# Performance work log

Measured on AMD Instinct MI355X. Metric: run time of the kernel, lower is better.

Reference implementation:

```python
import jax, jax.numpy as jnp
import numpy as np

B, D, H = 8, 512, 8
HD = D // H            # 64 head dim
NS, NT = 8192, 4096    # search / template points
ATTN_EPS = 1e-6
LN_EPS = 1e-5


def layer_norm(x, g, b):
    m = jnp.mean(x, axis=-1, keepdims=True)
    v = jnp.mean((x - m) ** 2, axis=-1, keepdims=True)
    return (x - m) * jax.lax.rsqrt(v + LN_EPS) * g + b


def setup_inputs() -> dict:
    key = jax.random.key(0)
    ks = jax.random.split(key, 20)
    s = 0.02
    return {
        "search_feat": jax.random.normal(ks[0], (B, D, NS), jnp.float32),
        "search_xyz": jax.random.uniform(ks[1], (B, NS, 3), jnp.float32),
        "template_feat": jax.random.normal(ks[2], (B, D, NT), jnp.float32),
        "template_xyz": jax.random.uniform(ks[3], (B, NT, 3), jnp.float32),
        "pos_w1": jax.random.normal(ks[4], (3, D), jnp.float32) * s,
        "pos_b1": jnp.zeros((D,), jnp.float32),
        "pos_w2": jax.random.normal(ks[5], (D, D), jnp.float32) * s,
        "pos_b2": jnp.zeros((D,), jnp.float32),
        "wq": jax.random.normal(ks[6], (D, D), jnp.float32) * s,
        "wk": jax.random.normal(ks[7], (D, D), jnp.float32) * s,
        "wv": jax.random.normal(ks[8], (D, D), jnp.float32) * s,
        "w_merge": jax.random.normal(ks[9], (D, D), jnp.float32) * s,
        "mlp_w1": jax.random.normal(ks[10], (2 * D, 2 * D), jnp.float32) * s,
        "mlp_w2": jax.random.normal(ks[11], (2 * D, D), jnp.float32) * s,
        "ln1_g": jnp.ones((D,), jnp.float32),
        "ln1_b": jnp.zeros((D,), jnp.float32),
        "ln2_g": jnp.ones((D,), jnp.float32),
        "ln2_b": jnp.zeros((D,), jnp.float32),
    }


def reference(search_feat, search_xyz, template_feat, template_xyz,
              pos_w1, pos_b1, pos_w2, pos_b2, wq, wk, wv, w_merge,
              mlp_w1, mlp_w2, ln1_g, ln1_b, ln2_g, ln2_b):
    bs = search_feat.shape[0]
    sf = jnp.transpose(search_feat, (0, 2, 1))    # [B, Ns, D]
    tf = jnp.transpose(template_feat, (0, 2, 1))  # [B, Nt, D]

    # positional MLP on template coordinates
    pos = jax.nn.relu(template_xyz @ pos_w1 + pos_b1) @ pos_w2 + pos_b2
    tf_pos = tf + pos

    q = (sf @ wq).reshape(bs, NS, H, HD)
    k = (tf @ wk).reshape(bs, NT, H, HD)
    v = (tf_pos @ wv).reshape(bs, NT, H, HD)

    # LoFTR-style linear attention: phi(x) = elu(x) + 1
    Q = jax.nn.elu(q) + 1.0
    K = jax.nn.elu(k) + 1.0
    v_len = v.shape[1]
    v_n = v / v_len
    KV = jnp.einsum("bshd,bshv->bhdv", K, v_n)                 # [B,H,d,d]
    Z = 1.0 / (jnp.einsum("blhd,bhd->blh", Q, K.sum(axis=1)) + ATTN_EPS)
    msg = jnp.einsum("blhd,bhdv->blhv", Q, KV) * Z[..., None] * v_len

    msg = msg.reshape(bs, NS, H * HD) @ w_merge
    msg = layer_norm(msg, ln1_g, ln1_b)
    cat = jnp.concatenate([sf, msg], axis=2)                    # [B,Ns,2D]
    msg = jax.nn.relu(cat @ mlp_w1) @ mlp_w2
    msg = layer_norm(msg, ln2_g, ln2_b)
    return jnp.transpose(sf + msg, (0, 2, 1))                   # [B,D,Ns]
```

## Files before the change

kernel.cpp:

```cpp
#include <hip/hip_runtime.h>
#include <stdint.h>
#include <stddef.h>


using ushort_t = unsigned short;
using short8 = __attribute__((ext_vector_type(8))) short;
using f32x4  = __attribute__((ext_vector_type(4))) float;

#define DEVI __device__ __forceinline__

DEVI float b2f(unsigned short u) {
    unsigned v = ((unsigned)u) << 16;
    return __builtin_bit_cast(float, v);
}
DEVI unsigned short f2b(float x) {
    unsigned u = __builtin_bit_cast(unsigned, x);
    u += 0x7FFFu + ((u >> 16) & 1u);
    return (unsigned short)(u >> 16);
}
DEVI void gload16(const void* g, void* l) {
    __builtin_amdgcn_global_load_lds(
        (const __attribute__((address_space(1))) unsigned*)g,
        (__attribute__((address_space(3))) unsigned*)l, 16, 0, 0);
}

template <int EPI>
__global__ __launch_bounds__(512, 2)
void gemm_bf16(const ushort_t* __restrict__ A0, const ushort_t* __restrict__ A1,
               const ushort_t* __restrict__ Wt, ushort_t* __restrict__ C,
               const float* __restrict__ bias, const ushort_t* __restrict__ addm,
               int N, int K, int K0, int lda0, int lda1, int nn)
{
    __shared__ ushort_t As[2][256 * 64];
    __shared__ ushort_t Bs[2][256 * 64];
    const int tid = threadIdx.x;
    const int cpx = gridDim.x >> 3;
    const int lid = (blockIdx.x & 7) * cpx + (blockIdx.x >> 3);
    const int m0 = (lid / nn) * 256;
    const int n0 = (lid % nn) * 256;
    const int w = tid >> 6, l = tid & 63;
    const int wm = (w >> 2) * 128;
    const int wn = (w & 3) * 64;
    const int lr = l & 15, lg = l >> 4;
    const int srow = tid >> 3;
    const int sck  = (tid & 7) ^ (srow & 7);
    const int nk = K / 64;

    f32x4 accA[4][4] = {};
    f32x4 accB[4][4] = {};

    auto stageA = [&](int kt, int buf) {
        const int kb = kt * 64;
        const ushort_t* p; int ld;
        if (kb < K0) { p = A0 + (size_t)m0 * lda0 + kb; ld = lda0; }
        else         { p = A1 + (size_t)m0 * lda1 + (kb - K0); ld = lda1; }
        p += (size_t)srow * ld + sck * 8;
#pragma unroll
        for (int j = 0; j < 4; j++)
            gload16(p + (size_t)(j * 64) * ld,
                    (void*)(&As[buf][j * 4096] + tid * 8));
    };
    auto stageB = [&](int kt, int buf) {
        const ushort_t* p = Wt + (size_t)(n0 + srow) * K + kt * 64 + sck * 8;
#pragma unroll
        for (int j = 0; j < 4; j++)
            gload16(p + (size_t)(j * 64) * K,
                    (void*)(&Bs[buf][j * 4096] + tid * 8));
    };

    short8 aP[4], aQ[4], aR[4], b0[4], b1[4];

    auto ldA = [&](short8 (&dst)[4], int mh, int ks, int cb) {
#pragma unroll
        for (int mf = 0; mf < 4; mf++) {
            const int r = wm + mh * 64 + mf * 16 + lr;
            dst[mf] = *(const short8*)&As[cb][r * 64 + ((ks * 4 + lg) ^ (r & 7)) * 8];
        }
    };
    auto ldB = [&](short8 (&dst)[4], int ks, int cb) {
#pragma unroll
        for (int nf = 0; nf < 4; nf++) {
            const int r = wn + nf * 16 + lr;
            dst[nf] = *(const short8*)&Bs[cb][r * 64 + ((ks * 4 + lg) ^ (r & 7)) * 8];
        }
    };
    auto MM = [&](f32x4 (&ac)[4][4], short8 (&af)[4], short8 (&bf)[4]) {
        __builtin_amdgcn_s_setprio(1);
#pragma unroll
        for (int mf = 0; mf < 4; mf++)
#pragma unroll
            for (int nf = 0; nf < 4; nf++)
                ac[mf][nf] = __builtin_amdgcn_mfma_f32_16x16x32_bf16(
                    af[mf], bf[nf], ac[mf][nf], 0, 0, 0);
        __builtin_amdgcn_s_setprio(0);
    };

    stageA(0, 0); stageB(0, 0);
    asm volatile("s_waitcnt vmcnt(0)" ::: "memory");
    __builtin_amdgcn_s_barrier();
    ldA(aP, 0, 0, 0); ldB(b0, 0, 0);

    for (int t = 0; t < nk; ++t) {
        const int cur = t & 1;
        const bool pre = (t + 1) < nk;
        ldA(aQ, 1, 0, cur); ldB(b1, 1, cur);
        if (pre) stageA(t + 1, cur ^ 1);
        MM(accA, aP, b0);
        ldA(aR, 0, 1, cur);
        if (pre) stageB(t + 1, cur ^ 1);
        MM(accB, aQ, b0);
        ldA(aP, 1, 1, cur);
        MM(accA, aR, b1);
        MM(accB, aP, b1);
        if (pre) {
            asm volatile("s_waitcnt vmcnt(0)" ::: "memory");
            __builtin_amdgcn_s_barrier();
            ldA(aP, 0, 0, cur ^ 1); ldB(b0, 0, cur ^ 1);
        }
    }

#pragma unroll
    for (int mf = 0; mf < 4; mf++) {
#pragma unroll
        for (int i = 0; i < 4; i++) {
            const int mA = m0 + wm + mf * 16 + lg * 4 + i;
            const int mB = mA + 64;
#pragma unroll
            for (int nf = 0; nf < 4; nf++) {
                const int n = n0 + wn + nf * 16 + lr;
                float x = accA[mf][nf][i];
                float y = accB[mf][nf][i];
                if constexpr (EPI == 1) {
                    x = x > 0.f ? x + 1.f : __expf(x);
                    y = y > 0.f ? y + 1.f : __expf(y);
                }
                if constexpr (EPI == 2) {
                    x += bias[n] + b2f(addm[(size_t)mA * N + n]);
                    y += bias[n] + b2f(addm[(size_t)mB * N + n]);
                }
                if constexpr (EPI == 3) { x = fmaxf(x, 0.f); y = fmaxf(y, 0.f); }
                C[(size_t)mA * N + n] = f2b(x);
                C[(size_t)mB * N + n] = f2b(y);
            }
        }
    }
}

__global__ __launch_bounds__(512, 2)
void gemm_proj(const ushort_t* __restrict__ sfT, const ushort_t* __restrict__ tfT,
               const ushort_t* __restrict__ P1,
               const ushort_t* __restrict__ wqT, const ushort_t* __restrict__ wkT,
               const ushort_t* __restrict__ pw2T,
               ushort_t* __restrict__ Qp, ushort_t* __restrict__ Kp,
               ushort_t* __restrict__ tfpos, const float* __restrict__ pos_b2)
{
    __shared__ ushort_t As[2][256 * 64];
    __shared__ ushort_t Bs[2][256 * 64];
    const int tid = threadIdx.x;
    const int cpx = gridDim.x >> 3;
    const int lid = (blockIdx.x & 7) * cpx + (blockIdx.x >> 3);
    const ushort_t* A0; const ushort_t* Wt; ushort_t* C; int loc; bool doElu;
    if (lid < 512)      { loc = lid;       A0 = sfT; Wt = wqT;  C = Qp;    doElu = true; }
    else if (lid < 768) { loc = lid - 512; A0 = tfT; Wt = wkT;  C = Kp;    doElu = true; }
    else                { loc = lid - 768; A0 = P1;  Wt = pw2T; C = tfpos; doElu = false; }
    const int m0 = (loc >> 1) * 256;
    const int n0 = (loc & 1) * 256;
    const int w = tid >> 6, l = tid & 63;
    const int wm = (w >> 2) * 128;
    const int wn = (w & 3) * 64;
    const int lr = l & 15, lg = l >> 4;
    const int srow = tid >> 3;
    const int sck  = (tid & 7) ^ (srow & 7);
    const int nk = 8;

    f32x4 accA[4][4] = {};
    f32x4 accB[4][4] = {};

    auto stageA = [&](int kt, int buf) {
        const ushort_t* p = A0 + (size_t)(m0 + srow) * 512 + kt * 64 + sck * 8;
#pragma unroll
        for (int j = 0; j < 4; j++)
            gload16(p + (size_t)(j * 64) * 512,
                    (void*)(&As[buf][j * 4096] + tid * 8));
    };
    auto stageB = [&](int kt, int buf) {
        const ushort_t* p = Wt + (size_t)(n0 + srow) * 512 + kt * 64 + sck * 8;
#pragma unroll
        for (int j = 0; j < 4; j++)
            gload16(p + (size_t)(j * 64) * 512,
                    (void*)(&Bs[buf][j * 4096] + tid * 8));
    };

    short8 aP[4], aQ[4], aR[4], b0[4], b1[4];

    auto ldA = [&](short8 (&dst)[4], int mh, int ks, int cb) {
#pragma unroll
        for (int mf = 0; mf < 4; mf++) {
            const int r = wm + mh * 64 + mf * 16 + lr;
            dst[mf] = *(const short8*)&As[cb][r * 64 + ((ks * 4 + lg) ^ (r & 7)) * 8];
        }
    };
    auto ldB = [&](short8 (&dst)[4], int ks, int cb) {
#pragma unroll
        for (int nf = 0; nf < 4; nf++) {
            const int r = wn + nf * 16 + lr;
            dst[nf] = *(const short8*)&Bs[cb][r * 64 + ((ks * 4 + lg) ^ (r & 7)) * 8];
        }
    };
    auto MM = [&](f32x4 (&ac)[4][4], short8 (&af)[4], short8 (&bf)[4]) {
        __builtin_amdgcn_s_setprio(1);
#pragma unroll
        for (int mf = 0; mf < 4; mf++)
#pragma unroll
            for (int nf = 0; nf < 4; nf++)
                ac[mf][nf] = __builtin_amdgcn_mfma_f32_16x16x32_bf16(
                    af[mf], bf[nf], ac[mf][nf], 0, 0, 0);
        __builtin_amdgcn_s_setprio(0);
    };

    stageA(0, 0); stageB(0, 0);
    asm volatile("s_waitcnt vmcnt(0)" ::: "memory");
    __builtin_amdgcn_s_barrier();
    ldA(aP, 0, 0, 0); ldB(b0, 0, 0);

    for (int t = 0; t < nk; ++t) {
        const int cur = t & 1;
        const bool pre = (t + 1) < nk;
        ldA(aQ, 1, 0, cur); ldB(b1, 1, cur);
        if (pre) stageA(t + 1, cur ^ 1);
        MM(accA, aP, b0);
        ldA(aR, 0, 1, cur);
        if (pre) stageB(t + 1, cur ^ 1);
        MM(accB, aQ, b0);
        ldA(aP, 1, 1, cur);
        MM(accA, aR, b1);
        MM(accB, aP, b1);
        if (pre) {
            asm volatile("s_waitcnt vmcnt(0)" ::: "memory");
            __builtin_amdgcn_s_barrier();
            ldA(aP, 0, 0, cur ^ 1); ldB(b0, 0, cur ^ 1);
        }
    }

#pragma unroll
    for (int mf = 0; mf < 4; mf++) {
#pragma unroll
        for (int i = 0; i < 4; i++) {
            const int mA = m0 + wm + mf * 16 + lg * 4 + i;
            const int mB = mA + 64;
#pragma unroll
            for (int nf = 0; nf < 4; nf++) {
                const int n = n0 + wn + nf * 16 + lr;
                float x = accA[mf][nf][i];
                float y = accB[mf][nf][i];
                if (doElu) {
                    x = x > 0.f ? x + 1.f : __expf(x);
                    y = y > 0.f ? y + 1.f : __expf(y);
                } else {
                    x += pos_b2[n] + b2f(tfT[(size_t)mA * 512 + n]);
                    y += pos_b2[n] + b2f(tfT[(size_t)mB * 512 + n]);
                }
                C[(size_t)mA * 512 + n] = f2b(x);
                C[(size_t)mB * 512 + n] = f2b(y);
            }
        }
    }
}

__global__ __launch_bounds__(256)
void prep(const float* __restrict__ sfeat, const float* __restrict__ tfeat,
          const float* __restrict__ xyz, const float* __restrict__ pw1,
          const float* __restrict__ pb1,
          const float* wq, const float* wk, const float* wv, const float* wm,
          const float* pw2, const float* w1, const float* w2,
          ushort_t* sfT, ushort_t* tfT, ushort_t* P1,
          ushort_t* wqT, ushort_t* wkT, ushort_t* wvT, ushort_t* wmT,
          ushort_t* pw2T, ushort_t* w1T, ushort_t* w2T)
{
    const int bid = blockIdx.x;
    const int t = threadIdx.x;
    if (bid >= 12992) {
        const int m = (bid - 12992) * 4 + (t >> 6);
        const int n0 = (t & 63) * 8;
        const float x = xyz[m * 3 + 0], y = xyz[m * 3 + 1], z = xyz[m * 3 + 2];
        short8 o;
#pragma unroll
        for (int j = 0; j < 8; j++) {
            const int n = n0 + j;
            float v = x * pw1[n] + y * pw1[512 + n] + z * pw1[1024 + n] + pb1[n];
            o[j] = (short)f2b(fmaxf(v, 0.f));
        }
        *(short8*)&P1[(size_t)m * 512 + n0] = o;
        return;
    }
    __shared__ float tile[64][65];
    const float* src; ushort_t* dst; int R, Cc, c0, r0;
    if (bid < 8192) {
        const int b = bid >> 10, rem = bid & 1023;
        src = sfeat + (size_t)b * 512 * 8192; dst = sfT + (size_t)b * 512 * 8192;
        R = 512; Cc = 8192; c0 = (rem & 127) * 64; r0 = (rem >> 7) * 64;
    } else if (bid < 12288) {
        const int lcl = bid - 8192; const int b = lcl >> 9, rem = lcl & 511;
        src = tfeat + (size_t)b * 512 * 4096; dst = tfT + (size_t)b * 512 * 4096;
        R = 512; Cc = 4096; c0 = (rem & 63) * 64; r0 = (rem >> 6) * 64;
    } else {
        const int lcl = bid - 12288;
        if (lcl < 320) {
            const int wsel = lcl >> 6, local = lcl & 63;
            const float* srcs[5] = {wq, wk, wv, wm, pw2};
            ushort_t* dsts[5] = {wqT, wkT, wvT, wmT, pw2T};
            src = srcs[wsel]; dst = dsts[wsel];
            R = 512; Cc = 512; c0 = (local & 7) * 64; r0 = (local >> 3) * 64;
        } else if (lcl < 576) {
            const int local = lcl - 320;
            src = w1; dst = w1T; R = 1024; Cc = 1024;
            c0 = (local & 15) * 64; r0 = (local >> 4) * 64;
        } else {
            const int local = lcl - 576;
            src = w2; dst = w2T; R = 1024; Cc = 512;
            c0 = (local & 7) * 64; r0 = (local >> 3) * 64;
        }
    }
#pragma unroll
    for (int i = 0; i < 4; i++) {
        const int r = (t >> 4) + i * 16;
        const int c = (t & 15) * 4;
        const float4 v = *(const float4*)&src[(size_t)(r0 + r) * Cc + c0 + c];
        tile[r][c + 0] = v.x; tile[r][c + 1] = v.y;
        tile[r][c + 2] = v.z; tile[r][c + 3] = v.w;
    }
    __syncthreads();
#pragma unroll
    for (int i = 0; i < 2; i++) {
        const int c = (t >> 3) + i * 32;
        const int rs = (t & 7) * 8;
        short8 o;
#pragma unroll
        for (int j = 0; j < 8; j++) o[j] = (short)f2b(tile[rs + j][c]);
        *(short8*)&dst[(size_t)(c0 + c) * R + r0 + rs] = o;
    }
}

__global__ __launch_bounds__(256)
void kv_partial(const ushort_t* __restrict__ Kp, const ushort_t* __restrict__ V,
                float* __restrict__ KVp, float* __restrict__ Ksp)
{
    __shared__ ushort_t Ks[256 * 64];
    __shared__ ushort_t Vs[256 * 64];
    const int t = threadIdx.x;
    const int sp = blockIdx.x, h = blockIdx.y, b = blockIdx.z;
    const int d0 = t >> 2, e0 = (t & 3) * 16;
    const int srow = t >> 3, scol = (t & 7) * 8;
    float acc[16] = {};
    float ksum = 0.f;
    for (int c = 0; c < 2; c++) {
        if (c) __syncthreads();
        const size_t sbase = (size_t)b * 4096 + sp * 512 + c * 256;
#pragma unroll
        for (int i = 0; i < 8; i++) {
            const size_t go = (sbase + i * 32 + srow) * 512 + h * 64 + scol;
            gload16(Kp + go, (void*)(&Ks[i * 2048] + t * 8));
            gload16(V + go, (void*)(&Vs[i * 2048] + t * 8));
        }
        __syncthreads();
        for (int s = 0; s < 256; s++) {
            const float k = b2f(Ks[s * 64 + d0]);
            if ((t & 3) == 0) ksum += k;
            const short8 v0 = *(const short8*)&Vs[s * 64 + e0];
            const short8 v1 = *(const short8*)&Vs[s * 64 + e0 + 8];
#pragma unroll
            for (int j = 0; j < 8; j++) {
                acc[j]     += k * b2f((unsigned short)v0[j]);
                acc[8 + j] += k * b2f((unsigned short)v1[j]);
            }
        }
    }
    const int bh = b * 8 + h;
    float* kvo = KVp + (((size_t)sp * 64 + bh) * 64 + d0) * 64 + e0;
#pragma unroll
    for (int j = 0; j < 16; j++) kvo[j] = acc[j];
    if ((t & 3) == 0) Ksp[((size_t)sp * 64 + bh) * 64 + d0] = ksum;
}

__global__ __launch_bounds__(256)
void kv_finalize(const float* __restrict__ KVp, const float* __restrict__ Ksp,
                 ushort_t* __restrict__ KVt)
{
    const int bh = blockIdx.x, t = threadIdx.x;
    ushort_t* o = KVt + (size_t)bh * 5120;
#pragma unroll
    for (int i = 0; i < 16; i++) {
        const int idx = i * 256 + t;
        const int e = idx >> 6, d = idx & 63;
        float s = 0.f;
#pragma unroll
        for (int sp = 0; sp < 8; sp++)
            s += KVp[(((size_t)sp * 64 + bh) * 64 + d) * 64 + e];
        o[idx] = f2b(s);
    }
    if (t < 64) {
        float s = 0.f;
#pragma unroll
        for (int sp = 0; sp < 8; sp++) s += Ksp[((size_t)sp * 64 + bh) * 64 + t];
        o[4096 + t] = f2b(s);
    }
    for (int idx = 4160 + t; idx < 5120; idx += 256) o[idx] = 0;
}

__global__ __launch_bounds__(256, 2)
void attn_apply(const ushort_t* __restrict__ Qp, const ushort_t* __restrict__ KVt,
                ushort_t* __restrict__ msg1)
{
    __shared__ ushort_t As[256 * 64];
    __shared__ ushort_t Bs[80 * 64];
    const int t = threadIdx.x;
    const int ch = blockIdx.x, h = blockIdx.y, b = blockIdx.z;
    const int w = t >> 6, l = t & 63;
    const int lr = l & 15, lg = l >> 4;
    const int row0 = ch * 256;
    const int srow = t >> 3;
    const int sc = ((t & 7) ^ (srow & 7)) * 8;
    const ushort_t* kv = KVt + (size_t)(b * 8 + h) * 5120;
#pragma unroll
    for (int i = 0; i < 2; i++)
        gload16(kv + (size_t)(i * 32 + srow) * 64 + sc,
                (void*)(&Bs[i * 2048] + t * 8));
    if (t < 128)
        gload16(kv + (size_t)(64 + srow) * 64 + sc,
                (void*)(&Bs[4096] + t * 8));
    const ushort_t* qb = Qp + ((size_t)b * 8192 + row0) * 512 + h * 64;
#pragma unroll
    for (int i = 0; i < 8; i++)
        gload16(qb + (size_t)(i * 32 + srow) * 512 + sc,
                (void*)(&As[i * 2048] + t * 8));
    __syncthreads();
    f32x4 acc[4][5] = {};
    const int wr = w * 64;
#pragma unroll
    for (int ks = 0; ks < 2; ks++) {
        const int kswz = ((ks * 4 + lg) ^ (lr & 7)) * 8;
        short8 a[4], bb[5];
#pragma unroll
        for (int mf = 0; mf < 4; mf++)
            a[mf] = *(const short8*)&As[(wr + mf * 16 + lr) * 64 + kswz];
#pragma unroll
        for (int nf = 0; nf < 5; nf++)
            bb[nf] = *(const short8*)&Bs[(nf * 16 + lr) * 64 + kswz];
#pragma unroll
        for (int mf = 0; mf < 4; mf++)
#pragma unroll
            for (int nf = 0; nf < 5; nf++)
                acc[mf][nf] = __builtin_amdgcn_mfma_f32_16x16x32_bf16(
                    a[mf], bb[nf], acc[mf][nf], 0, 0, 0);
    }
#pragma unroll
    for (int mf = 0; mf < 4; mf++) {
#pragma unroll
        for (int i = 0; i < 4; i++) {
            const int m = row0 + wr + mf * 16 + lg * 4 + i;
            const float zden = __shfl(acc[mf][4][i], (l & 48));
            const float z = 1.f / (zden + 1e-6f);
#pragma unroll
            for (int nf = 0; nf < 4; nf++) {
                const int e = nf * 16 + lr;
                msg1[((size_t)b * 8192 + m) * 512 + h * 64 + e] =
                    f2b(acc[mf][nf][i] * z);
            }
        }
    }
}

__global__ __launch_bounds__(256)
void layer_norm_k(ushort_t* __restrict__ X, const float* __restrict__ g,
                  const float* __restrict__ bta)
{
    const int t = threadIdx.x;
    const int row = blockIdx.x * 4 + (t >> 6);
    const int l = t & 63;
    ushort_t* x = X + (size_t)row * 512;
    const short8 v = *(const short8*)&x[l * 8];
    float f[8];
    float s = 0.f;
#pragma unroll
    for (int j = 0; j < 8; j++) { f[j] = b2f((unsigned short)v[j]); s += f[j]; }
#pragma unroll
    for (int o = 32; o > 0; o >>= 1) s += __shfl_xor(s, o);
    const float mean = s * (1.f / 512.f);
    float vs = 0.f;
#pragma unroll
    for (int j = 0; j < 8; j++) { const float d = f[j] - mean; vs += d * d; }
#pragma unroll
    for (int o = 32; o > 0; o >>= 1) vs += __shfl_xor(vs, o);
    const float rstd = rsqrtf(vs * (1.f / 512.f) + 1e-5f);
    short8 ov;
#pragma unroll
    for (int j = 0; j < 8; j++) {
        const int c = l * 8 + j;
        ov[j] = (short)f2b((f[j] - mean) * rstd * g[c] + bta[c]);
    }
    *(short8*)&x[l * 8] = ov;
}

__global__ __launch_bounds__(256)
void ln2_final(const ushort_t* __restrict__ outp, const ushort_t* __restrict__ sfT,
               const float* __restrict__ g, const float* __restrict__ bta,
               float* __restrict__ out)
{
    __shared__ ushort_t tile[64][514];
    const int t = threadIdx.x;
    const int ns0 = blockIdx.x * 64, b = blockIdx.y;
    const int w = t >> 6, l = t & 63;
#pragma unroll
    for (int rr = 0; rr < 16; rr++) {
        const int r = w * 16 + rr;
        const size_t grow = (size_t)b * 8192 + ns0 + r;
        const short8 v = *(const short8*)&outp[grow * 512 + l * 8];
        float f[8];
        float s = 0.f;
#pragma unroll
        for (int j = 0; j < 8; j++) { f[j] = b2f((unsigned short)v[j]); s += f[j]; }
#pragma unroll
        for (int o = 32; o > 0; o >>= 1) s += __shfl_xor(s, o);
        const float mean = s * (1.f / 512.f);
        float vs = 0.f;
#pragma unroll
        for (int j = 0; j < 8; j++) { const float d = f[j] - mean; vs += d * d; }
#pragma unroll
        for (int o = 32; o > 0; o >>= 1) vs += __shfl_xor(vs, o);
        const float rstd = rsqrtf(vs * (1.f / 512.f) + 1e-5f);
        const short8 sv = *(const short8*)&sfT[grow * 512 + l * 8];
        short8 ov;
#pragma unroll
        for (int j = 0; j < 8; j++) {
            const int c = l * 8 + j;
            ov[j] = (short)f2b(b2f((unsigned short)sv[j]) +
                               (f[j] - mean) * rstd * g[c] + bta[c]);
        }
        *(short8*)&tile[r][l * 8] = ov;
    }
    __syncthreads();
#pragma unroll
    for (int i = 0; i < 32; i++) {
        const int d = (t >> 4) + i * 16;
        const int nss = (t & 15) * 4;
        float4 o;
        o.x = b2f(tile[nss + 0][d]);
        o.y = b2f(tile[nss + 1][d]);
        o.z = b2f(tile[nss + 2][d]);
        o.w = b2f(tile[nss + 3][d]);
        *(float4*)&out[((size_t)b * 512 + d) * 8192 + ns0 + nss] = o;
    }
}

extern "C" void kernel_launch(void* const* d_in, const int* in_sizes, int n_in,
                              void* d_out, int out_size, void* d_ws, size_t ws_size,
                              hipStream_t stream)
{
    (void)in_sizes; (void)n_in; (void)out_size; (void)ws_size;
    const float* search_feat   = (const float*)d_in[0];
    const float* template_feat = (const float*)d_in[2];
    const float* template_xyz  = (const float*)d_in[3];
    const float* pos_w1  = (const float*)d_in[4];
    const float* pos_b1  = (const float*)d_in[5];
    const float* pos_w2  = (const float*)d_in[6];
    const float* pos_b2  = (const float*)d_in[7];
    const float* wq      = (const float*)d_in[8];
    const float* wk      = (const float*)d_in[9];
    const float* wv      = (const float*)d_in[10];
    const float* w_merge = (const float*)d_in[11];
    const float* mlp_w1  = (const float*)d_in[12];
    const float* mlp_w2  = (const float*)d_in[13];
    const float* ln1_g   = (const float*)d_in[14];
    const float* ln1_b   = (const float*)d_in[15];
    const float* ln2_g   = (const float*)d_in[16];
    const float* ln2_b   = (const float*)d_in[17];
    float* out = (float*)d_out;

    char* ws = (char*)d_ws;
    ushort_t* sfT    = (ushort_t*)(ws + 0);
    ushort_t* Qp     = (ushort_t*)(ws + 67108864);
    ushort_t* tfT    = (ushort_t*)(ws + 134217728);
    ushort_t* Kp     = (ushort_t*)(ws + 167772160);
    ushort_t* msg2   = (ushort_t*)(ws + 134217728);
    ushort_t* P1     = (ushort_t*)(ws + 201326592);
    ushort_t* Vv     = (ushort_t*)(ws + 201326592);
    ushort_t* tfpos  = (ushort_t*)(ws + 234881024);
    ushort_t* msg1   = (ushort_t*)(ws + 268435456);
    ushort_t* hidden = (ushort_t*)(ws + 201326592);
    ushort_t* outp   = Qp;
    ushort_t* wqT  = (ushort_t*)(ws + 335544320);
    ushort_t* wkT  = (ushort_t*)(ws + 336068608);
    ushort_t* wvT  = (ushort_t*)(ws + 336592896);
    ushort_t* wmT  = (ushort_t*)(ws + 337117184);
    ushort_t* pw2T = (ushort_t*)(ws + 337641472);
    ushort_t* w1T  = (ushort_t*)(ws + 338165760);
    ushort_t* w2T  = (ushort_t*)(ws + 340262912);
    float*    KVp  = (float*)(ws + 268435456);
    float*    Ksp  = (float*)(ws + 276824064);
    ushort_t* KVt  = (ushort_t*)(ws + 345571328);

    prep<<<dim3(21184), 256, 0, stream>>>(
        search_feat, template_feat, template_xyz, pos_w1, pos_b1,
        wq, wk, wv, w_merge, pos_w2, mlp_w1, mlp_w2,
        sfT, tfT, P1, wqT, wkT, wvT, wmT, pw2T, w1T, w2T);
    gemm_proj<<<dim3(1024), 512, 0, stream>>>(sfT, tfT, P1, wqT, wkT, pw2T,
                                              Qp, Kp, tfpos, pos_b2);
    gemm_bf16<0><<<dim3(256), 512, 0, stream>>>(tfpos, nullptr, wvT, Vv,
                                                nullptr, nullptr, 512, 512, 512, 512, 0, 2);
    kv_partial<<<dim3(8, 8, 8), 256, 0, stream>>>(Kp, Vv, KVp, Ksp);
    kv_finalize<<<dim3(64), 256, 0, stream>>>(KVp, Ksp, KVt);
    attn_apply<<<dim3(32, 8, 8), 256, 0, stream>>>(Qp, KVt, msg1);
    gemm_bf16<0><<<dim3(512), 512, 0, stream>>>(msg1, nullptr, wmT, msg2,
                                                nullptr, nullptr, 512, 512, 512, 512, 0, 2);
    layer_norm_k<<<dim3(16384), 256, 0, stream>>>(msg2, ln1_g, ln1_b);
    gemm_bf16<3><<<dim3(1024), 512, 0, stream>>>(sfT, msg2, w1T, hidden,
                                                 nullptr, nullptr, 1024, 1024, 512, 512, 512, 4);
    gemm_bf16<0><<<dim3(512), 512, 0, stream>>>(hidden, nullptr, w2T, outp,
                                                nullptr, nullptr, 512, 1024, 1024, 1024, 0, 2);
    ln2_final<<<dim3(128, 8), 256, 0, stream>>>(outp, sfT, ln2_g, ln2_b, out);
}
```

Before: 708.1 us.

## Replace 256x256 double-buffered GEMMs with single-buffered 128x128 tiles

Every GEMM kernel, the fused projection one included, moves from 256x256 tiles with 512 threads and double-buffered LDS prefetch to 128x128 tiles with 256 threads and a single LDS buffer. Grids grow four- to eightfold and launch bounds now allow four blocks per CU. The aim is more parallelism and better wave occupancy for these fairly small GEMMs. In exchange, each tile does less operand reuse and global loads no longer overlap with MFMA work inside a block, so the code relies on other resident blocks to hide that latency.

```diff
diff --git a/kernel.cpp b/kernel.cpp
--- a/kernel.cpp
+++ b/kernel.cpp
@@ -25,128 +25,89 @@
 }
 
 template <int EPI>
-__global__ __launch_bounds__(512, 2)
-void gemm_bf16(const ushort_t* __restrict__ A0, const ushort_t* __restrict__ A1,
-               const ushort_t* __restrict__ Wt, ushort_t* __restrict__ C,
-               const float* __restrict__ bias, const ushort_t* __restrict__ addm,
-               int N, int K, int K0, int lda0, int lda1, int nn)
-{
-    __shared__ ushort_t As[2][256 * 64];
-    __shared__ ushort_t Bs[2][256 * 64];
+__global__ __launch_bounds__(256, 4)
+void gemm128(const ushort_t* __restrict__ A0, const ushort_t* __restrict__ A1,
+             const ushort_t* __restrict__ Wt, ushort_t* __restrict__ C,
+             const float* __restrict__ bias, const ushort_t* __restrict__ addm,
+             int N, int K, int K0, int lda0, int lda1, int nn)
+{
+    __shared__ ushort_t As[128 * 64];
+    __shared__ ushort_t Bs[128 * 64];
     const int tid = threadIdx.x;
     const int cpx = gridDim.x >> 3;
     const int lid = (blockIdx.x & 7) * cpx + (blockIdx.x >> 3);
-    const int m0 = (lid / nn) * 256;
-    const int n0 = (lid % nn) * 256;
+    const int m0 = (lid / nn) * 128;
+    const int n0 = (lid % nn) * 128;
     const int w = tid >> 6, l = tid & 63;
-    const int wm = (w >> 2) * 128;
-    const int wn = (w & 3) * 64;
+    const int wm = (w >> 1) * 64, wn = (w & 1) * 64;
     const int lr = l & 15, lg = l >> 4;
     const int srow = tid >> 3;
     const int sck  = (tid & 7) ^ (srow & 7);
     const int nk = K / 64;
 
-    f32x4 accA[4][4] = {};
-    f32x4 accB[4][4] = {};
-
-    auto stageA = [&](int kt, int buf) {
-        const int kb = kt * 64;
-        const ushort_t* p; int ld;
-        if (kb < K0) { p = A0 + (size_t)m0 * lda0 + kb; ld = lda0; }
-        else         { p = A1 + (size_t)m0 * lda1 + (kb - K0); ld = lda1; }
-        p += (size_t)srow * ld + sck * 8;
-#pragma unroll
-        for (int j = 0; j < 4; j++)
-            gload16(p + (size_t)(j * 64) * ld,
-                    (void*)(&As[buf][j * 4096] + tid * 8));
-    };
-    auto stageB = [&](int kt, int buf) {
-        const ushort_t* p = Wt + (size_t)(n0 + srow) * K + kt * 64 + sck * 8;
-#pragma unroll
-        for (int j = 0; j < 4; j++)
-            gload16(p + (size_t)(j * 64) * K,
-                    (void*)(&Bs[buf][j * 4096] + tid * 8));
-    };
-
-    short8 aP[4], aQ[4], aR[4], b0[4], b1[4];
-
-    auto ldA = [&](short8 (&dst)[4], int mh, int ks, int cb) {
-#pragma unroll
-        for (int mf = 0; mf < 4; mf++) {
-            const int r = wm + mh * 64 + mf * 16 + lr;
-            dst[mf] = *(const short8*)&As[cb][r * 64 + ((ks * 4 + lg) ^ (r & 7)) * 8];
-        }
-    };
-    auto ldB = [&](short8 (&dst)[4], int ks, int cb) {
-#pragma unroll
-        for (int nf = 0; nf < 4; nf++) {
-            const int r = wn + nf * 16 + lr;
-            dst[nf] = *(const short8*)&Bs[cb][r * 64 + ((ks * 4 + lg) ^ (r & 7)) * 8];
-        }
-    };
-    auto MM = [&](f32x4 (&ac)[4][4], short8 (&af)[4], short8 (&bf)[4]) {
-        __builtin_amdgcn_s_setprio(1);
-#pragma unroll
-        for (int mf = 0; mf < 4; mf++)
-#pragma unroll
-            for (int nf = 0; nf < 4; nf++)
-                ac[mf][nf] = __builtin_amdgcn_mfma_f32_16x16x32_bf16(
-                    af[mf], bf[nf], ac[mf][nf], 0, 0, 0);
-        __builtin_amdgcn_s_setprio(0);
-    };
-
-    stageA(0, 0); stageB(0, 0);
-    asm volatile("s_waitcnt vmcnt(0)" ::: "memory");
-    __builtin_amdgcn_s_barrier();
-    ldA(aP, 0, 0, 0); ldB(b0, 0, 0);
+    f32x4 acc[4][4] = {};
 
     for (int t = 0; t < nk; ++t) {
-        const int cur = t & 1;
-        const bool pre = (t + 1) < nk;
-        ldA(aQ, 1, 0, cur); ldB(b1, 1, cur);
-        if (pre) stageA(t + 1, cur ^ 1);
-        MM(accA, aP, b0);
-        ldA(aR, 0, 1, cur);
-        if (pre) stageB(t + 1, cur ^ 1);
-        MM(accB, aQ, b0);
-        ldA(aP, 1, 1, cur);
-        MM(accA, aR, b1);
-        MM(accB, aP, b1);
-        if (pre) {
-            asm volatile("s_waitcnt vmcnt(0)" ::: "memory");
-            __builtin_amdgcn_s_barrier();
-            ldA(aP, 0, 0, cur ^ 1); ldB(b0, 0, cur ^ 1);
-        }
+        const int kb = t * 64;
+        {
+            const ushort_t* p; int ld;
+            if (kb < K0) { p = A0 + (size_t)m0 * lda0 + kb; ld = lda0; }
+            else         { p = A1 + (size_t)m0 * lda1 + (kb - K0); ld = lda1; }
+            p += (size_t)srow * ld + sck * 8;
+#pragma unroll
+            for (int j = 0; j < 4; j++)
+                gload16(p + (size_t)(j * 32) * ld, (void*)(&As[j * 2048] + tid * 8));
+            const ushort_t* q = Wt + (size_t)(n0 + srow) * K + kb + sck * 8;
+#pragma unroll
+            for (int j = 0; j < 4; j++)
+                gload16(q + (size_t)(j * 32) * K, (void*)(&Bs[j * 2048] + tid * 8));
+        }
+        asm volatile("s_waitcnt vmcnt(0)" ::: "memory");
+        __builtin_amdgcn_s_barrier();
+#pragma unroll
+        for (int ks = 0; ks < 2; ks++) {
+            short8 a[4], b[4];
+#pragma unroll
+            for (int mf = 0; mf < 4; mf++) {
+                const int r = wm + mf * 16 + lr;
+                a[mf] = *(const short8*)&As[r * 64 + ((ks * 4 + lg) ^ (r & 7)) * 8];
+            }
+#pragma unroll
+            for (int nf = 0; nf < 4; nf++) {
+                const int r = wn + nf * 16 + lr;
+                b[nf] = *(const short8*)&Bs[r * 64 + ((ks * 4 + lg) ^ (r & 7)) * 8];
+            }
+            __builtin_amdgcn_s_setprio(1);
+#pragma unroll
+            for (int mf = 0; mf < 4; mf++)
+#pragma unroll
+                for (int nf = 0; nf < 4; nf++)
+                    acc[mf][nf] = __builtin_amdgcn_mfma_f32_16x16x32_bf16(
+                        a[mf], b[nf], acc[mf][nf], 0, 0, 0);
+            __builtin_amdgcn_s_setprio(0);
+        }
+        __builtin_amdgcn_s_barrier();
     }
 
 #pragma unroll
     for (int mf = 0; mf < 4; mf++) {
 #pragma unroll
         for (int i = 0; i < 4; i++) {
-            const int mA = m0 + wm + mf * 16 + lg * 4 + i;
-            const int mB = mA + 64;
+            const int m = m0 + wm + mf * 16 + lg * 4 + i;
 #pragma unroll
             for (int nf = 0; nf < 4; nf++) {
                 const int n = n0 + wn + nf * 16 + lr;
-                float x = accA[mf][nf][i];
-                float y = accB[mf][nf][i];
-                if constexpr (EPI == 1) {
-                    x = x > 0.f ? x + 1.f : __expf(x);
-                    y = y > 0.f ? y + 1.f : __expf(y);
-                }
-                if constexpr (EPI == 2) {
-                    x += bias[n] + b2f(addm[(size_t)mA * N + n]);
-                    y += bias[n] + b2f(addm[(size_t)mB * N + n]);
-                }
-                if constexpr (EPI == 3) { x = fmaxf(x, 0.f); y = fmaxf(y, 0.f); }
-                C[(size_t)mA * N + n] = f2b(x);
-                C[(size_t)mB * N + n] = f2b(y);
-            }
-        }
-    }
-}
-
-__global__ __launch_bounds__(512, 2)
+                float x = acc[mf][nf][i];
+                if constexpr (EPI == 1) { x = x > 0.f ? x + 1.f : __expf(x); }
+                if constexpr (EPI == 2) { x += bias[n] + b2f(addm[(size_t)m * N + n]); }
+                if constexpr (EPI == 3) { x = fmaxf(x, 0.f); }
+                C[(size_t)m * N + n] = f2b(x);
+            }
+        }
+    }
+}
+
+__global__ __launch_bounds__(256, 4)
 void gemm_proj(const ushort_t* __restrict__ sfT, const ushort_t* __restrict__ tfT,
                const ushort_t* __restrict__ P1,
                const ushort_t* __restrict__ wqT, const ushort_t* __restrict__ wkT,
@@ -154,114 +115,79 @@
                ushort_t* __restrict__ Qp, ushort_t* __restrict__ Kp,
                ushort_t* __restrict__ tfpos, const float* __restrict__ pos_b2)
 {
-    __shared__ ushort_t As[2][256 * 64];
-    __shared__ ushort_t Bs[2][256 * 64];
+    __shared__ ushort_t As[128 * 64];
+    __shared__ ushort_t Bs[128 * 64];
     const int tid = threadIdx.x;
     const int cpx = gridDim.x >> 3;
     const int lid = (blockIdx.x & 7) * cpx + (blockIdx.x >> 3);
     const ushort_t* A0; const ushort_t* Wt; ushort_t* C; int loc; bool doElu;
-    if (lid < 512)      { loc = lid;       A0 = sfT; Wt = wqT;  C = Qp;    doElu = true; }
-    else if (lid < 768) { loc = lid - 512; A0 = tfT; Wt = wkT;  C = Kp;    doElu = true; }
-    else                { loc = lid - 768; A0 = P1;  Wt = pw2T; C = tfpos; doElu = false; }
-    const int m0 = (loc >> 1) * 256;
-    const int n0 = (loc & 1) * 256;
+    if (lid < 2048)      { loc = lid;        A0 = sfT; Wt = wqT;  C = Qp;    doElu = true; }
+    else if (lid < 3072) { loc = lid - 2048; A0 = tfT; Wt = wkT;  C = Kp;    doElu = true; }
+    else                 { loc = lid - 3072; A0 = P1;  Wt = pw2T; C = tfpos; doElu = false; }
+    const int m0 = (loc >> 2) * 128;
+    const int n0 = (loc & 3) * 128;
     const int w = tid >> 6, l = tid & 63;
-    const int wm = (w >> 2) * 128;
-    const int wn = (w & 3) * 64;
+    const int wm = (w >> 1) * 64, wn = (w & 1) * 64;
     const int lr = l & 15, lg = l >> 4;
     const int srow = tid >> 3;
     const int sck  = (tid & 7) ^ (srow & 7);
-    const int nk = 8;
-
-    f32x4 accA[4][4] = {};
-    f32x4 accB[4][4] = {};
-
-    auto stageA = [&](int kt, int buf) {
-        const ushort_t* p = A0 + (size_t)(m0 + srow) * 512 + kt * 64 + sck * 8;
-#pragma unroll
-        for (int j = 0; j < 4; j++)
-            gload16(p + (size_t)(j * 64) * 512,
-                    (void*)(&As[buf][j * 4096] + tid * 8));
-    };
-    auto stageB = [&](int kt, int buf) {
-        const ushort_t* p = Wt + (size_t)(n0 + srow) * 512 + kt * 64 + sck * 8;
-#pragma unroll
-        for (int j = 0; j < 4; j++)
-            gload16(p + (size_t)(j * 64) * 512,
-                    (void*)(&Bs[buf][j * 4096] + tid * 8));
-    };
-
-    short8 aP[4], aQ[4], aR[4], b0[4], b1[4];
-
-    auto ldA = [&](short8 (&dst)[4], int mh, int ks, int cb) {
-#pragma unroll
-        for (int mf = 0; mf < 4; mf++) {
-            const int r = wm + mh * 64 + mf * 16 + lr;
-            dst[mf] = *(const short8*)&As[cb][r * 64 + ((ks * 4 + lg) ^ (r & 7)) * 8];
-        }
-    };
-    auto ldB = [&](short8 (&dst)[4], int ks, int cb) {
-#pragma unroll
-        for (int nf = 0; nf < 4; nf++) {
-            const int r = wn + nf * 16 + lr;
-            dst[nf] = *(const short8*)&Bs[cb][r * 64 + ((ks * 4 + lg) ^ (r & 7)) * 8];
-        }
-    };
-    auto MM = [&](f32x4 (&ac)[4][4], short8 (&af)[4], short8 (&bf)[4]) {
-        __builtin_amdgcn_s_setprio(1);
-#pragma unroll
-        for (int mf = 0; mf < 4; mf++)
-#pragma unroll
-            for (int nf = 0; nf < 4; nf++)
-                ac[mf][nf] = __builtin_amdgcn_mfma_f32_16x16x32_bf16(
-                    af[mf], bf[nf], ac[mf][nf], 0, 0, 0);
-        __builtin_amdgcn_s_setprio(0);
-    };
-
-    stageA(0, 0); stageB(0, 0);
-    asm volatile("s_waitcnt vmcnt(0)" ::: "memory");
-    __builtin_amdgcn_s_barrier();
-    ldA(aP, 0, 0, 0); ldB(b0, 0, 0);
-
-    for (int t = 0; t < nk; ++t) {
-        const int cur = t & 1;
-        const bool pre = (t + 1) < nk;
-        ldA(aQ, 1, 0, cur); ldB(b1, 1, cur);
-        if (pre) stageA(t + 1, cur ^ 1);
-        MM(accA, aP, b0);
-        ldA(aR, 0, 1, cur);
-        if (pre) stageB(t + 1, cur ^ 1);
-        MM(accB, aQ, b0);
-        ldA(aP, 1, 1, cur);
-        MM(accA, aR, b1);
-        MM(accB, aP, b1);
-        if (pre) {
-            asm volatile("s_waitcnt vmcnt(0)" ::: "memory");
-            __builtin_amdgcn_s_barrier();
-            ldA(aP, 0, 0, cur ^ 1); ldB(b0, 0, cur ^ 1);
-        }
+
+    f32x4 acc[4][4] = {};
+
+    for (int t = 0; t < 8; ++t) {
+        const int kb = t * 64;
+        {
+            const ushort_t* p = A0 + (size_t)(m0 + srow) * 512 + kb + sck * 8;
+#pragma unroll
+            for (int j = 0; j < 4; j++)
+                gload16(p + (size_t)(j * 32) * 512, (void*)(&As[j * 2048] + tid * 8));
+            const ushort_t* q = Wt + (size_t)(n0 + srow) * 512 + kb + sck * 8;
+#pragma unroll
+            for (int j = 0; j < 4; j++)
+                gload16(q + (size_t)(j * 32) * 512, (void*)(&Bs[j * 2048] + tid * 8));
+        }
+        asm volatile("s_waitcnt vmcnt(0)" ::: "memory");
+        __builtin_amdgcn_s_barrier();
+#pragma unroll
+        for (int ks = 0; ks < 2; ks++) {
+            short8 a[4], b[4];
+#pragma unroll
+            for (int mf = 0; mf < 4; mf++) {
+                const int r = wm + mf * 16 + lr;
+                a[mf] = *(const short8*)&As[r * 64 + ((ks * 4 + lg) ^ (r & 7)) * 8];
+            }
+#pragma unroll
+            for (int nf = 0; nf < 4; nf++) {
+                const int r = wn + nf * 16 + lr;
+                b[nf] = *(const short8*)&Bs[r * 64 + ((ks * 4 + lg) ^ (r & 7)) * 8];
+            }
+            __builtin_amdgcn_s_setprio(1);
+#pragma unroll
+            for (int mf = 0; mf < 4; mf++)
+#pragma unroll
+                for (int nf = 0; nf < 4; nf++)
+                    acc[mf][nf] = __builtin_amdgcn_mfma_f32_16x16x32_bf16(
+                        a[mf], b[nf], acc[mf][nf], 0, 0, 0);
+            __builtin_amdgcn_s_setprio(0);
+        }
+        __builtin_amdgcn_s_barrier();
     }
 
 #pragma unroll
     for (int mf = 0; mf < 4; mf++) {
 #pragma unroll
         for (int i = 0; i < 4; i++) {
-            const int mA = m0 + wm + mf * 16 + lg * 4 + i;
-            const int mB = mA + 64;
+            const int m = m0 + wm + mf * 16 + lg * 4 + i;
 #pragma unroll
             for (int nf = 0; nf < 4; nf++) {
                 const int n = n0 + wn + nf * 16 + lr;
-                float x = accA[mf][nf][i];
-                float y = accB[mf][nf][i];
+                float x = acc[mf][nf][i];
                 if (doElu) {
                     x = x > 0.f ? x + 1.f : __expf(x);
-                    y = y > 0.f ? y + 1.f : __expf(y);
                 } else {
-                    x += pos_b2[n] + b2f(tfT[(size_t)mA * 512 + n]);
-                    y += pos_b2[n] + b2f(tfT[(size_t)mB * 512 + n]);
+                    x += pos_b2[n] + b2f(tfT[(size_t)m * 512 + n]);
                 }
-                C[(size_t)mA * 512 + n] = f2b(x);
-                C[(size_t)mB * 512 + n] = f2b(y);
+                C[(size_t)m * 512 + n] = f2b(x);
             }
         }
     }
@@ -603,19 +529,19 @@
         search_feat, template_feat, template_xyz, pos_w1, pos_b1,
         wq, wk, wv, w_merge, pos_w2, mlp_w1, mlp_w2,
         sfT, tfT, P1, wqT, wkT, wvT, wmT, pw2T, w1T, w2T);
-    gemm_proj<<<dim3(1024), 512, 0, stream>>>(sfT, tfT, P1, wqT, wkT, pw2T,
+    gemm_proj<<<dim3(4096), 256, 0, stream>>>(sfT, tfT, P1, wqT, wkT, pw2T,
                                               Qp, Kp, tfpos, pos_b2);
-    gemm_bf16<0><<<dim3(256), 512, 0, stream>>>(tfpos, nullptr, wvT, Vv,
-                                                nullptr, nullptr, 512, 512, 512, 512, 0, 2);
+    gemm128<0><<<dim3(1024), 256, 0, stream>>>(tfpos, nullptr, wvT, Vv,
+                                               nullptr, nullptr, 512, 512, 512, 512, 0, 4);
     kv_partial<<<dim3(8, 8, 8), 256, 0, stream>>>(Kp, Vv, KVp, Ksp);
     kv_finalize<<<dim3(64), 256, 0, stream>>>(KVp, Ksp, KVt);
     attn_apply<<<dim3(32, 8, 8), 256, 0, stream>>>(Qp, KVt, msg1);
-    gemm_bf16<0><<<dim3(512), 512, 0, stream>>>(msg1, nullptr, wmT, msg2,
-                                                nullptr, nullptr, 512, 512, 512, 512, 0, 2);
+    gemm128<0><<<dim3(2048), 256, 0, stream>>>(msg1, nullptr, wmT, msg2,
+                                               nullptr, nullptr, 512, 512, 512, 512, 0, 4);
     layer_norm_k<<<dim3(16384), 256, 0, stream>>>(msg2, ln1_g, ln1_b);
-    gemm_bf16<3><<<dim3(1024), 512, 0, stream>>>(sfT, msg2, w1T, hidden,
-                                                 nullptr, nullptr, 1024, 1024, 512, 512, 512, 4);
-    gemm_bf16<0><<<dim3(512), 512, 0, stream>>>(hidden, nullptr, w2T, outp,
-                                                nullptr, nullptr, 512, 1024, 1024, 1024, 0, 2);
+    gemm128<3><<<dim3(4096), 256, 0, stream>>>(sfT, msg2, w1T, hidden,
+                                               nullptr, nullptr, 1024, 1024, 512, 512, 512, 8);
+    gemm128<0><<<dim3(2048), 256, 0, stream>>>(hidden, nullptr, w2T, outp,
+                                               nullptr, nullptr, 512, 1024, 1024, 1024, 0, 4);
     ln2_final<<<dim3(128, 8), 256, 0, stream>>>(outp, sfT, ln2_g, ln2_b, out);
 }
```

Result: faster. 658.5 us (-7.0%).
